# Kernel optimization log

Hardware: AMD Instinct MI355X
Metric: run time of the kernel (lower is better)

Reference implementation:

```python
import jax, jax.numpy as jnp
import numpy as np

NS = 100000   # served nodes
NI = 100000   # interfered nodes
E = 1000000   # edges per relation
D = 64        # 2 * Nt_num, Nt_num = 32
HM = 32       # message MLP hidden
HU = 16       # update MLP hidden


def _lin_init(key, fan_in, fan_out):
    s = 1.0 / np.sqrt(fan_in)
    kw, kb = jax.random.split(key)
    w = jax.random.uniform(kw, (fan_in, fan_out), jnp.float32, -s, s)
    b = jax.random.uniform(kb, (fan_out,), jnp.float32, -s, s)
    return w, b


def setup_inputs() -> dict:
    key = jax.random.key(0)
    ks = jax.random.split(key, 12)
    wm1, bm1 = _lin_init(ks[0], D, HM)
    wm2, bm2 = _lin_init(ks[1], HM, D)
    wu1, bu1 = _lin_init(ks[2], D, HU)
    wu2, bu2 = _lin_init(ks[3], HU, D)
    wo, bo = _lin_init(ks[4], D, D)
    edge_s2i = jnp.stack([
        jax.random.randint(ks[5], (E,), 0, NS),   # src in served
        jax.random.randint(ks[6], (E,), 0, NI),   # dst in interfered
    ]).astype(jnp.int64)
    edge_i2s = jnp.stack([
        jax.random.randint(ks[7], (E,), 0, NI),   # src in interfered
        jax.random.randint(ks[8], (E,), 0, NS),   # dst in served
    ]).astype(jnp.int64)
    return {
        "x_served": jax.random.normal(ks[9], (NS, D), jnp.float32),
        "x_interfered": jax.random.normal(ks[10], (NI, D), jnp.float32),
        "edge_s2i": edge_s2i,
        "edge_i2s": edge_i2s,
        "wm1": wm1, "bm1": bm1, "wm2": wm2, "bm2": bm2,
        "wu1": wu1, "bu1": bu1, "wu2": wu2, "bu2": bu2,
        "wo": wo, "bo": bo,
    }


def reference(x_served, x_interfered, edge_s2i, edge_i2s,
              wm1, bm1, wm2, bm2, wu1, bu1, wu2, bu2, wo, bo):
    def mlp_m(h):  # MLP([D, 32, D]): Lin+ReLU, Lin+ReLU
        return jax.nn.relu(jax.nn.relu(h @ wm1 + bm1) @ wm2 + bm2)

    def mlp_u(h):  # MLP([D, 16, D])
        return jax.nn.relu(jax.nn.relu(h @ wu1 + bu1) @ wu2 + bu2)

    def conv(x_src, edges, n_dst):
        # gather source node features per edge, per-edge message MLP
        msg = mlp_m(x_src[edges[0]])                    # [E, D]
        # scatter-sum into destination nodes
        agg = jax.ops.segment_sum(msg, edges[1], num_segments=n_dst)
        return mlp_u(agg)                               # [n_dst, D]

    xs, xi = x_served, x_interfered
    for _ in range(3):
        new_i = conv(xs, edge_s2i, NI)   # served -> interfered
        new_s = conv(xi, edge_i2s, NS)   # interfered -> served
        xs, xi = new_s, new_i
    # h2o on served: Lin + Tanh -> beamforming matrix
    return jnp.tanh(xs @ wo + bo)
```

## Files before the change

kernel.cpp:

```cpp
#include <hip/hip_runtime.h>
#include <hip/hip_fp16.h>
#include <math.h>

constexpr int D = 64;
constexpr int CAP = 48;
constexpr int RPB = 256;
constexpr int EPB = 4096;

typedef _Float16 half2_t __attribute__((ext_vector_type(2)));

__device__ inline float fdot2(unsigned a, unsigned b, float c){
    return __builtin_amdgcn_fdot2(__builtin_bit_cast(half2_t, a),
                                  __builtin_bit_cast(half2_t, b), c, false);
}

__device__ inline unsigned pack2(float lo, float hi){
    __half2 h = __floats2half2_rn(lo, hi);
    return *(unsigned*)&h;
}

__device__ inline void ld16u(const unsigned* base, unsigned* w){
    const uint4* p = (const uint4*)base;
    uint4 a = p[0], b = p[1], c = p[2], d = p[3];
    w[0]=a.x;  w[1]=a.y;  w[2]=a.z;  w[3]=a.w;
    w[4]=b.x;  w[5]=b.y;  w[6]=b.z;  w[7]=b.w;
    w[8]=c.x;  w[9]=c.y;  w[10]=c.z; w[11]=c.w;
    w[12]=d.x; w[13]=d.y; w[14]=d.z; w[15]=d.w;
}

__device__ inline void store_half8(__half* dst, const float* o){
    uint4 w;
    w.x = pack2(o[0], o[1]); w.y = pack2(o[2], o[3]);
    w.z = pack2(o[4], o[5]); w.w = pack2(o[6], o[7]);
    *((uint4*)dst) = w;
}

__device__ inline void load_half8(const __half* src, float* r){
    uint4 w = *((const uint4*)src);
    __half2* h = (__half2*)&w;
    float2 f0 = __half22float2(h[0]);
    float2 f1 = __half22float2(h[1]);
    float2 f2 = __half22float2(h[2]);
    float2 f3 = __half22float2(h[3]);
    r[0] = f0.x; r[1] = f0.y; r[2] = f1.x; r[3] = f1.y;
    r[4] = f2.x; r[5] = f2.y; r[6] = f3.x; r[7] = f3.y;
}


__global__ void __launch_bounds__(256) k_bucket_mlpm(
        const int* __restrict__ es2i, const int* __restrict__ ei2s, int E, int NI,
        int NBUK, int BSTRIDE,
        int* __restrict__ gcur, unsigned* __restrict__ buckets,
        const float* __restrict__ x,
        const float* __restrict__ wm1, const float* __restrict__ bm1,
        const float* __restrict__ wm2, const float* __restrict__ bm2,
        __half* __restrict__ y, int Nmlp, int nbEdge)
{
    __shared__ __align__(16) char smem[8704];
    int t = threadIdx.x;

    if ((int)blockIdx.x < nbEdge){
        int* hist = (int*)smem;
        int* base = (int*)(smem + 4096);
        for (int i = t; i < NBUK; i += 256) hist[i] = 0;
        __syncthreads();
        int e0 = blockIdx.x * EPB + t;
        int rr[16], ss[16];
        #pragma unroll
        for (int k = 0; k < 16; k++){
            int i = e0 + k*256;
            if (i < E){
                ss[k] = es2i[i];            rr[k] = es2i[E + i];
            } else if (i < 2*E){
                int j = i - E;
                ss[k] = ei2s[j];            rr[k] = NI + ei2s[E + j];
            } else rr[k] = -1;
        }
        #pragma unroll
        for (int k = 0; k < 16; k++)
            if (rr[k] >= 0) atomicAdd(&hist[rr[k] >> 8], 1);
        __syncthreads();
        for (int b = t; b < NBUK; b += 256){
            int h = hist[b];
            base[b] = h ? atomicAdd(&gcur[b], h) : 0;
        }
        __syncthreads();
        #pragma unroll
        for (int k = 0; k < 16; k++){
            if (rr[k] >= 0){
                int b = rr[k] >> 8;
                int p = atomicAdd(&base[b], 1);
                if (p < BSTRIDE)
                    buckets[(size_t)b*BSTRIDE + p] =
                        ((unsigned)(rr[k] & 255) << 24) | (unsigned)ss[k];
            }
        }
        return;
    }

    unsigned* w1p = (unsigned*)smem;
    unsigned* w2p = (unsigned*)(smem + 4096);
    float*    sb1 = (float*)(smem + 8192);
    float*    sb2 = (float*)(smem + 8320);
    for (int i = t; i < 1024; i += 256){ int kp=i>>5, j=i&31; w1p[i]=pack2(wm1[(2*kp)*32+j], wm1[(2*kp+1)*32+j]); }
    for (int i = t; i < 1024; i += 256){ int jp=i>>6, c=i&63; w2p[i]=pack2(wm2[(2*jp)*64+c], wm2[(2*jp+1)*64+c]); }
    if (t < 32) sb1[t] = bm1[t];
    if (t < 64) sb2[t] = bm2[t];
    __syncthreads();
    int n = ((int)blockIdx.x - nbEdge)*256 + t;
    if (n >= Nmlp) return;

    const float4* xp = (const float4*)(x + (size_t)n*D);
    unsigned xq[32];
    #pragma unroll
    for (int i = 0; i < 16; i++){
        float4 v = xp[i];
        xq[2*i]   = pack2(v.x, v.y);
        xq[2*i+1] = pack2(v.z, v.w);
    }
    float h[32];
    #pragma unroll
    for (int j = 0; j < 32; j++) h[j] = 0.f;
    #pragma unroll
    for (int kp = 0; kp < 32; kp++){
        unsigned xv = xq[kp];
        unsigned w[32];
        ld16u(&w1p[kp*32],      w);
        ld16u(&w1p[kp*32 + 16], w + 16);
        #pragma unroll
        for (int j = 0; j < 32; j++) h[j] = fdot2(xv, w[j], h[j]);
    }
    #pragma unroll
    for (int j = 0; j < 32; j++) h[j] = fmaxf(h[j] + sb1[j], 0.f);
    unsigned hh[16];
    #pragma unroll
    for (int jp = 0; jp < 16; jp++) hh[jp] = pack2(h[2*jp], h[2*jp+1]);

    __half* yrow = y + (size_t)n*D;
    #pragma unroll
    for (int c0 = 0; c0 < 64; c0 += 32){
        float o[32];
        #pragma unroll
        for (int c = 0; c < 32; c++) o[c] = sb2[c0 + c];
        #pragma unroll
        for (int jp = 0; jp < 16; jp++){
            unsigned hv = hh[jp];
            unsigned w[32];
            ld16u(&w2p[jp*64 + c0],      w);
            ld16u(&w2p[jp*64 + c0 + 16], w + 16);
            #pragma unroll
            for (int c = 0; c < 32; c++) o[c] = fdot2(hv, w[c], o[c]);
        }
        #pragma unroll
        for (int c = 0; c < 32; c++) o[c] = fmaxf(o[c], 0.f);
        store_half8(yrow + c0,      &o[0]);
        store_half8(yrow + c0 + 8,  &o[8]);
        store_half8(yrow + c0 + 16, &o[16]);
        store_half8(yrow + c0 + 24, &o[24]);
    }
}


__global__ void __launch_bounds__(512) k_scatter_lds(const int* __restrict__ gcur,
        const unsigned* __restrict__ buckets, int BSTRIDE, int NTOT,
        int* __restrict__ cnt, int* __restrict__ slots)
{
    __shared__ int lcnt[RPB];
    __shared__ int lslots[RPB*CAP];
    int t = threadIdx.x;
    int b = blockIdx.x;
    int r0 = b * RPB;
    int nrows = NTOT - r0; if (nrows > RPB) nrows = RPB;

    for (int i = t; i < RPB; i += 512) lcnt[i] = 0;
    __syncthreads();

    int n = gcur[b]; if (n > BSTRIDE) n = BSTRIDE;
    const unsigned* bp = buckets + (size_t)b*BSTRIDE;
    for (int k = t; k < n; k += 512){
        unsigned e = bp[k];
        int lr  = e >> 24;
        int src = e & 0xFFFFFF;
        int pos = atomicAdd(&lcnt[lr], 1);
        if (pos < CAP) lslots[lr*CAP + pos] = src;
    }
    __syncthreads();

    int4* gs = (int4*)(slots + (size_t)r0*CAP);
    const int4* ls = (const int4*)lslots;
    int n4 = nrows*CAP/4;
    for (int i = t; i < n4; i += 512) gs[i] = ls[i];
    for (int i = t; i < nrows; i += 512) cnt[r0 + i] = lcnt[i];
}


__global__ void __launch_bounds__(256) k_agg(const __half* __restrict__ M,
        const int* __restrict__ cnt, const int* __restrict__ slots,
        __half* __restrict__ agg, int N)
{
    int gid  = blockIdx.x*256 + threadIdx.x;
    int node = gid >> 6;
    if (node >= N) return;
    int lane = gid & 63;
    int sub  = lane >> 3;
    int fl   = lane & 7;
    int deg = cnt[node]; deg = deg < CAP ? deg : CAP;
    const int* row = slots + (size_t)node*CAP;
    float acc[8];
    #pragma unroll
    for (int i = 0; i < 8; i++) acc[i] = 0.f;
    for (int k = sub; k < deg; k += 8){
        int s = row[k];
        float v[8];
        load_half8(M + (size_t)s*D + fl*8, v);
        #pragma unroll
        for (int i = 0; i < 8; i++) acc[i] += v[i];
    }
    #pragma unroll
    for (int i = 0; i < 8; i++){
        acc[i] += __shfl_xor(acc[i], 8);
        acc[i] += __shfl_xor(acc[i], 16);
        acc[i] += __shfl_xor(acc[i], 32);
    }
    if (sub == 0) store_half8(agg + (size_t)node*D + fl*8, acc);
}


__global__ void __launch_bounds__(256) k_mlp_um(const __half* __restrict__ agg,
        const float* __restrict__ wu1, const float* __restrict__ bu1,
        const float* __restrict__ wu2, const float* __restrict__ bu2,
        const float* __restrict__ wm1, const float* __restrict__ bm1,
        const float* __restrict__ wm2, const float* __restrict__ bm2,
        __half* __restrict__ y, int N)
{
    __shared__ __align__(16) unsigned w1p[32*16];
    __shared__ __align__(16) unsigned w2p[8*64];
    __shared__ __align__(16) unsigned m1p[32*32];
    __shared__ __align__(16) unsigned m2p[16*64];
    __shared__ float sbu1[16], sbu2[64], sbm1[32], sbm2[64];
    int t = threadIdx.x;
    for (int i = t; i < 512;  i += 256){ int kp=i>>4, j=i&15; w1p[i]=pack2(wu1[(2*kp)*16+j], wu1[(2*kp+1)*16+j]); }
    for (int i = t; i < 512;  i += 256){ int jp=i>>6, c=i&63; w2p[i]=pack2(wu2[(2*jp)*64+c], wu2[(2*jp+1)*64+c]); }
    for (int i = t; i < 1024; i += 256){ int kp=i>>5, j=i&31; m1p[i]=pack2(wm1[(2*kp)*32+j], wm1[(2*kp+1)*32+j]); }
    for (int i = t; i < 1024; i += 256){ int kp=i>>6, c=i&63; m2p[i]=pack2(wm2[(2*kp)*64+c], wm2[(2*kp+1)*64+c]); }
    if (t < 16) sbu1[t] = bu1[t];
    if (t < 64) sbu2[t] = bu2[t];
    if (t < 32) sbm1[t] = bm1[t];
    if (t < 64) sbm2[t] = bm2[t];
    __syncthreads();
    int n = blockIdx.x*256 + t;
    if (n >= N) return;

    unsigned xq[32];
    {
        const uint4* p = (const uint4*)(agg + (size_t)n*D);
        #pragma unroll
        for (int i = 0; i < 8; i++){
            uint4 w = p[i];
            xq[4*i] = w.x; xq[4*i+1] = w.y; xq[4*i+2] = w.z; xq[4*i+3] = w.w;
        }
    }

    float h[16];
    #pragma unroll
    for (int j = 0; j < 16; j++) h[j] = 0.f;
    #pragma unroll
    for (int kp = 0; kp < 32; kp++){
        unsigned a = xq[kp];
        unsigned w[16];
        ld16u(&w1p[kp*16], w);
        #pragma unroll
        for (int j = 0; j < 16; j++) h[j] = fdot2(a, w[j], h[j]);
    }
    #pragma unroll
    for (int j = 0; j < 16; j++) h[j] = fmaxf(h[j] + sbu1[j], 0.f);
    unsigned hp[8];
    #pragma unroll
    for (int jp = 0; jp < 8; jp++) hp[jp] = pack2(h[2*jp], h[2*jp+1]);

    #pragma unroll
    for (int c0 = 0; c0 < 64; c0 += 32){
        float o[32];
        #pragma unroll
        for (int c = 0; c < 32; c++) o[c] = sbu2[c0 + c];
        #pragma unroll
        for (int jp = 0; jp < 8; jp++){
            unsigned a = hp[jp];
            unsigned w[32];
            ld16u(&w2p[jp*64 + c0],      w);
            ld16u(&w2p[jp*64 + c0 + 16], w + 16);
            #pragma unroll
            for (int c = 0; c < 32; c++) o[c] = fdot2(a, w[c], o[c]);
        }
        #pragma unroll
        for (int c = 0; c < 32; c += 2)
            xq[(c0 + c) >> 1] = pack2(fmaxf(o[c], 0.f), fmaxf(o[c+1], 0.f));
    }

    float hm[32];
    #pragma unroll
    for (int j = 0; j < 32; j++) hm[j] = 0.f;
    #pragma unroll
    for (int kp = 0; kp < 32; kp++){
        unsigned a = xq[kp];
        unsigned w[32];
        ld16u(&m1p[kp*32],      w);
        ld16u(&m1p[kp*32 + 16], w + 16);
        #pragma unroll
        for (int j = 0; j < 32; j++) hm[j] = fdot2(a, w[j], hm[j]);
    }
    #pragma unroll
    for (int j = 0; j < 32; j++) hm[j] = fmaxf(hm[j] + sbm1[j], 0.f);
    unsigned hq[16];
    #pragma unroll
    for (int jp = 0; jp < 16; jp++) hq[jp] = pack2(hm[2*jp], hm[2*jp+1]);

    __half* yrow = y + (size_t)n*D;
    #pragma unroll
    for (int c0 = 0; c0 < 64; c0 += 32){
        float o[32];
        #pragma unroll
        for (int c = 0; c < 32; c++) o[c] = sbm2[c0 + c];
        #pragma unroll
        for (int kp = 0; kp < 16; kp++){
            unsigned a = hq[kp];
            unsigned w[32];
            ld16u(&m2p[kp*64 + c0],      w);
            ld16u(&m2p[kp*64 + c0 + 16], w + 16);
            #pragma unroll
            for (int c = 0; c < 32; c++) o[c] = fdot2(a, w[c], o[c]);
        }
        #pragma unroll
        for (int c = 0; c < 32; c++) o[c] = fmaxf(o[c], 0.f);
        store_half8(yrow + c0,      &o[0]);
        store_half8(yrow + c0 + 8,  &o[8]);
        store_half8(yrow + c0 + 16, &o[16]);
        store_half8(yrow + c0 + 24, &o[24]);
    }
}


__device__ inline float fast_tanh(float x){
    float ax = fabsf(x);
    float e  = __expf(2.f*ax);
    float t  = 1.f - 2.f/(e + 1.f);
    return copysignf(t, x);
}

__global__ void __launch_bounds__(256) k_mlp_uo(const __half* __restrict__ agg,
        const float* __restrict__ wu1, const float* __restrict__ bu1,
        const float* __restrict__ wu2, const float* __restrict__ bu2,
        const float* __restrict__ wo,  const float* __restrict__ bo,
        float* __restrict__ out, int N)
{
    __shared__ __align__(16) unsigned w1p[32*16];
    __shared__ __align__(16) unsigned w2p[8*64];
    __shared__ __align__(16) unsigned wop[32*64];
    __shared__ float sbu1[16], sbu2[64], sbo[64];
    __shared__ float stage[256*65];
    int t = threadIdx.x;
    for (int i = t; i < 512;  i += 256){ int kp=i>>4, j=i&15; w1p[i]=pack2(wu1[(2*kp)*16+j], wu1[(2*kp+1)*16+j]); }
    for (int i = t; i < 512;  i += 256){ int jp=i>>6, c=i&63; w2p[i]=pack2(wu2[(2*jp)*64+c], wu2[(2*jp+1)*64+c]); }
    for (int i = t; i < 2048; i += 256){ int kp=i>>6, c=i&63; wop[i]=pack2(wo[(2*kp)*64+c], wo[(2*kp+1)*64+c]); }
    if (t < 16) sbu1[t] = bu1[t];
    if (t < 64) sbu2[t] = bu2[t];
    if (t < 64) sbo[t]  = bo[t];
    __syncthreads();
    int n = blockIdx.x*256 + t;

    if (n < N){
        unsigned xq[32];
        {
            const uint4* p = (const uint4*)(agg + (size_t)n*D);
            #pragma unroll
            for (int i = 0; i < 8; i++){
                uint4 w = p[i];
                xq[4*i] = w.x; xq[4*i+1] = w.y; xq[4*i+2] = w.z; xq[4*i+3] = w.w;
            }
        }

        float h[16];
        #pragma unroll
        for (int j = 0; j < 16; j++) h[j] = 0.f;
        #pragma unroll
        for (int kp = 0; kp < 32; kp++){
            unsigned a = xq[kp];
            unsigned w[16];
            ld16u(&w1p[kp*16], w);
            #pragma unroll
            for (int j = 0; j < 16; j++) h[j] = fdot2(a, w[j], h[j]);
        }
        #pragma unroll
        for (int j = 0; j < 16; j++) h[j] = fmaxf(h[j] + sbu1[j], 0.f);
        unsigned hp[8];
        #pragma unroll
        for (int jp = 0; jp < 8; jp++) hp[jp] = pack2(h[2*jp], h[2*jp+1]);

        #pragma unroll
        for (int c0 = 0; c0 < 64; c0 += 32){
            float o[32];
            #pragma unroll
            for (int c = 0; c < 32; c++) o[c] = sbu2[c0 + c];
            #pragma unroll
            for (int jp = 0; jp < 8; jp++){
                unsigned a = hp[jp];
                unsigned w[32];
                ld16u(&w2p[jp*64 + c0],      w);
                ld16u(&w2p[jp*64 + c0 + 16], w + 16);
                #pragma unroll
                for (int c = 0; c < 32; c++) o[c] = fdot2(a, w[c], o[c]);
            }
            #pragma unroll
            for (int c = 0; c < 32; c += 2)
                xq[(c0 + c) >> 1] = pack2(fmaxf(o[c], 0.f), fmaxf(o[c+1], 0.f));
        }

        float* srow = &stage[t*65];
        #pragma unroll
        for (int c0 = 0; c0 < 64; c0 += 32){
            float o[32];
            #pragma unroll
            for (int c = 0; c < 32; c++) o[c] = sbo[c0 + c];
            #pragma unroll
            for (int kp = 0; kp < 32; kp++){
                unsigned a = xq[kp];
                unsigned w[32];
                ld16u(&wop[kp*64 + c0],      w);
                ld16u(&wop[kp*64 + c0 + 16], w + 16);
                #pragma unroll
                for (int c = 0; c < 32; c++) o[c] = fdot2(a, w[c], o[c]);
            }
            #pragma unroll
            for (int c = 0; c < 32; c++) srow[c0 + c] = fast_tanh(o[c]);
        }
    }
    __syncthreads();

    size_t blkbase = (size_t)blockIdx.x * 256 * 64;
    size_t limit   = (size_t)N * 64;
    #pragma unroll
    for (int k = 0; k < 16; k++){
        int f = k*256 + t;
        size_t e = blkbase + (size_t)f*4;
        if (e < limit){
            int ln = f >> 4;
            int c4 = (f & 15) * 4;
            float4 v;
            v.x = stage[ln*65 + c4];
            v.y = stage[ln*65 + c4 + 1];
            v.z = stage[ln*65 + c4 + 2];
            v.w = stage[ln*65 + c4 + 3];
            *((float4*)(out + e)) = v;
        }
    }
}


extern "C" void kernel_launch(void* const* d_in, const int* in_sizes, int n_in,
                              void* d_out, int out_size, void* d_ws, size_t ws_size,
                              hipStream_t stream)
{
    const float* x_interfered = (const float*)d_in[1];
    const int*   e_s2i        = (const int*)d_in[2];
    const int*   e_i2s        = (const int*)d_in[3];
    const float* wm1 = (const float*)d_in[4];  const float* bm1 = (const float*)d_in[5];
    const float* wm2 = (const float*)d_in[6];  const float* bm2 = (const float*)d_in[7];
    const float* wu1 = (const float*)d_in[8];  const float* bu1 = (const float*)d_in[9];
    const float* wu2 = (const float*)d_in[10]; const float* bu2 = (const float*)d_in[11];
    const float* wo  = (const float*)d_in[12]; const float* bo  = (const float*)d_in[13];

    const int NS = in_sizes[0] / D;
    const int NI = in_sizes[1] / D;
    const int E  = in_sizes[2] / 2;
    const int NMAX = (NS > NI) ? NS : NI;
    const int NTOT = NI + NS;

    const int NBUK = ((NTOT - 1) >> 8) + 1;
    int avg = (2*E) / NBUK;
    const int BSTRIDE = ((2*avg) + 1023) & ~1023;

    char* p = (char*)d_ws;
    auto alloc = [&](size_t bytes) -> void* {
        void* r = (void*)p;
        p += (bytes + 255) & ~(size_t)255;
        return r;
    };
    __half*   M      = (__half*)alloc((size_t)NMAX*D*2);
    __half*   AGG    = (__half*)alloc((size_t)NMAX*D*2);
    int*      cnt    = (int*)alloc((size_t)NTOT*4);
    int*      gcur   = (int*)alloc((size_t)NBUK*4);
    int*      slots  = (int*)alloc((size_t)NTOT*CAP*4);
    unsigned* buckets= (unsigned*)alloc((size_t)NBUK*BSTRIDE*4);
    (void)ws_size; (void)n_in; (void)out_size;

    const int* cnt_i = cnt;
    const int* cnt_s = cnt + NI;
    const int* slots_i = slots;
    const int* slots_s = slots + (size_t)NI*CAP;

    hipMemsetAsync(gcur, 0, (size_t)NBUK*4, stream);

    const int nbEdge = (2*E + EPB - 1)/EPB;
    const int nbMlp  = (NI + 255)/256;
    k_bucket_mlpm<<<nbEdge + nbMlp, 256, 0, stream>>>(
        e_s2i, e_i2s, E, NI, NBUK, BSTRIDE, gcur, buckets,
        x_interfered, wm1, bm1, wm2, bm2, M, NI, nbEdge);
    k_scatter_lds<<<NBUK, 512, 0, stream>>>(gcur, buckets, BSTRIDE, NTOT, cnt, slots);

    k_agg<<<((size_t)NS*64 + 255)/256, 256, 0, stream>>>(M, cnt_s, slots_s, AGG, NS);
    k_mlp_um<<<(NS + 255)/256, 256, 0, stream>>>(AGG, wu1, bu1, wu2, bu2,
                                               wm1, bm1, wm2, bm2, M, NS);
    k_agg<<<((size_t)NI*64 + 255)/256, 256, 0, stream>>>(M, cnt_i, slots_i, AGG, NI);
    k_mlp_um<<<(NI + 255)/256, 256, 0, stream>>>(AGG, wu1, bu1, wu2, bu2,
                                               wm1, bm1, wm2, bm2, M, NI);
    k_agg<<<((size_t)NS*64 + 255)/256, 256, 0, stream>>>(M, cnt_s, slots_s, AGG, NS);
    k_mlp_uo<<<(NS + 255)/256, 256, 0, stream>>>(AGG, wu1, bu1, wu2, bu2,
                                               wo, bo, (float*)d_out, NS);
}
```

Baseline: 250.8 us.

## Use MFMA 16x16x32 f16 for fused update+message MLP kernel

Rewrites k_mlp_um so each wavefront processes 16 nodes at a time with MFMA matrix instructions instead of per-thread fdot2 loops. Weights are held in registers as MFMA B fragments, and intermediate activations go through small per-wave LDS tiles to re-layout them as A fragments. Each block now covers 128 nodes in two tiles, and the grid size is adjusted to match. This is meant to cut VALU work and LDS weight re-reads, at the cost of LDS round-trips between layers and no sync between the per-wave LDS writes and reads.

```diff
diff --git a/kernel.cpp b/kernel.cpp
--- a/kernel.cpp
+++ b/kernel.cpp
@@ -8,6 +8,8 @@
 constexpr int EPB = 4096;
 
 typedef _Float16 half2_t __attribute__((ext_vector_type(2)));
+typedef _Float16 f16x8 __attribute__((ext_vector_type(8)));
+typedef float f32x4 __attribute__((ext_vector_type(4)));
 
 __device__ inline float fdot2(unsigned a, unsigned b, float c){
     return __builtin_amdgcn_fdot2(__builtin_bit_cast(half2_t, a),
@@ -233,109 +235,121 @@
         const float* __restrict__ wm2, const float* __restrict__ bm2,
         __half* __restrict__ y, int N)
 {
-    __shared__ __align__(16) unsigned w1p[32*16];
-    __shared__ __align__(16) unsigned w2p[8*64];
-    __shared__ __align__(16) unsigned m1p[32*32];
-    __shared__ __align__(16) unsigned m2p[16*64];
-    __shared__ float sbu1[16], sbu2[64], sbm1[32], sbm2[64];
-    int t = threadIdx.x;
-    for (int i = t; i < 512;  i += 256){ int kp=i>>4, j=i&15; w1p[i]=pack2(wu1[(2*kp)*16+j], wu1[(2*kp+1)*16+j]); }
-    for (int i = t; i < 512;  i += 256){ int jp=i>>6, c=i&63; w2p[i]=pack2(wu2[(2*jp)*64+c], wu2[(2*jp+1)*64+c]); }
-    for (int i = t; i < 1024; i += 256){ int kp=i>>5, j=i&31; m1p[i]=pack2(wm1[(2*kp)*32+j], wm1[(2*kp+1)*32+j]); }
-    for (int i = t; i < 1024; i += 256){ int kp=i>>6, c=i&63; m2p[i]=pack2(wm2[(2*kp)*64+c], wm2[(2*kp+1)*64+c]); }
-    if (t < 16) sbu1[t] = bu1[t];
-    if (t < 64) sbu2[t] = bu2[t];
-    if (t < 32) sbm1[t] = bm1[t];
-    if (t < 64) sbm2[t] = bm2[t];
-    __syncthreads();
-    int n = blockIdx.x*256 + t;
-    if (n >= N) return;
-
-    unsigned xq[32];
-    {
-        const uint4* p = (const uint4*)(agg + (size_t)n*D);
+    __shared__ float  lds_h [4][16][20];
+    __shared__ float  lds_y [4][16][68];
+    __shared__ float  lds_hm[4][16][36];
+    __shared__ __half lds_m [4][16][72];
+
+    int t  = threadIdx.x;
+    int wv = t >> 6, l = t & 63;
+    int m  = l & 15, g = l >> 4;
+
+    f16x8 Bu1[2], Bu2[4], Bm1[2][2], Bm2[4];
+    #pragma unroll
+    for (int kt = 0; kt < 2; kt++)
+        #pragma unroll
+        for (int i = 0; i < 8; i++)
+            Bu1[kt][i] = (_Float16)wu1[(kt*32 + 8*g + i)*16 + m];
+    #pragma unroll
+    for (int jb = 0; jb < 4; jb++)
         #pragma unroll
         for (int i = 0; i < 8; i++){
-            uint4 w = p[i];
-            xq[4*i] = w.x; xq[4*i+1] = w.y; xq[4*i+2] = w.z; xq[4*i+3] = w.w;
-        }
-    }
-
-    float h[16];
-    #pragma unroll
-    for (int j = 0; j < 16; j++) h[j] = 0.f;
-    #pragma unroll
-    for (int kp = 0; kp < 32; kp++){
-        unsigned a = xq[kp];
-        unsigned w[16];
-        ld16u(&w1p[kp*16], w);
-        #pragma unroll
-        for (int j = 0; j < 16; j++) h[j] = fdot2(a, w[j], h[j]);
-    }
-    #pragma unroll
-    for (int j = 0; j < 16; j++) h[j] = fmaxf(h[j] + sbu1[j], 0.f);
-    unsigned hp[8];
-    #pragma unroll
-    for (int jp = 0; jp < 8; jp++) hp[jp] = pack2(h[2*jp], h[2*jp+1]);
-
-    #pragma unroll
-    for (int c0 = 0; c0 < 64; c0 += 32){
-        float o[32];
-        #pragma unroll
-        for (int c = 0; c < 32; c++) o[c] = sbu2[c0 + c];
-        #pragma unroll
-        for (int jp = 0; jp < 8; jp++){
-            unsigned a = hp[jp];
-            unsigned w[32];
-            ld16u(&w2p[jp*64 + c0],      w);
-            ld16u(&w2p[jp*64 + c0 + 16], w + 16);
-            #pragma unroll
-            for (int c = 0; c < 32; c++) o[c] = fdot2(a, w[c], o[c]);
-        }
-        #pragma unroll
-        for (int c = 0; c < 32; c += 2)
-            xq[(c0 + c) >> 1] = pack2(fmaxf(o[c], 0.f), fmaxf(o[c+1], 0.f));
-    }
-
-    float hm[32];
-    #pragma unroll
-    for (int j = 0; j < 32; j++) hm[j] = 0.f;
-    #pragma unroll
-    for (int kp = 0; kp < 32; kp++){
-        unsigned a = xq[kp];
-        unsigned w[32];
-        ld16u(&m1p[kp*32],      w);
-        ld16u(&m1p[kp*32 + 16], w + 16);
-        #pragma unroll
-        for (int j = 0; j < 32; j++) hm[j] = fdot2(a, w[j], hm[j]);
-    }
-    #pragma unroll
-    for (int j = 0; j < 32; j++) hm[j] = fmaxf(hm[j] + sbm1[j], 0.f);
-    unsigned hq[16];
-    #pragma unroll
-    for (int jp = 0; jp < 16; jp++) hq[jp] = pack2(hm[2*jp], hm[2*jp+1]);
-
-    __half* yrow = y + (size_t)n*D;
-    #pragma unroll
-    for (int c0 = 0; c0 < 64; c0 += 32){
-        float o[32];
-        #pragma unroll
-        for (int c = 0; c < 32; c++) o[c] = sbm2[c0 + c];
-        #pragma unroll
-        for (int kp = 0; kp < 16; kp++){
-            unsigned a = hq[kp];
-            unsigned w[32];
-            ld16u(&m2p[kp*64 + c0],      w);
-            ld16u(&m2p[kp*64 + c0 + 16], w + 16);
-            #pragma unroll
-            for (int c = 0; c < 32; c++) o[c] = fdot2(a, w[c], o[c]);
-        }
-        #pragma unroll
-        for (int c = 0; c < 32; c++) o[c] = fmaxf(o[c], 0.f);
-        store_half8(yrow + c0,      &o[0]);
-        store_half8(yrow + c0 + 8,  &o[8]);
-        store_half8(yrow + c0 + 16, &o[16]);
-        store_half8(yrow + c0 + 24, &o[24]);
+            int k = 8*g + i;
+            Bu2[jb][i] = (k < 16) ? (_Float16)wu2[k*64 + jb*16 + m] : (_Float16)0.f;
+        }
+    #pragma unroll
+    for (int kt = 0; kt < 2; kt++)
+        #pragma unroll
+        for (int nt = 0; nt < 2; nt++)
+            #pragma unroll
+            for (int i = 0; i < 8; i++)
+                Bm1[kt][nt][i] = (_Float16)wm1[(kt*32 + 8*g + i)*32 + nt*16 + m];
+    #pragma unroll
+    for (int jb = 0; jb < 4; jb++)
+        #pragma unroll
+        for (int i = 0; i < 8; i++)
+            Bm2[jb][i] = (_Float16)wm2[(8*g + i)*64 + jb*16 + m];
+
+    float bu1v = bu1[m];
+    float bu2v[4], bm2v[4], bm1v[2];
+    #pragma unroll
+    for (int jb = 0; jb < 4; jb++){ bu2v[jb] = bu2[jb*16 + m]; bm2v[jb] = bm2[jb*16 + m]; }
+    #pragma unroll
+    for (int nt = 0; nt < 2; nt++) bm1v[nt] = bm1[nt*16 + m];
+
+    #pragma unroll
+    for (int tile = 0; tile < 2; tile++){
+        int nb = blockIdx.x*128 + tile*64 + wv*16;
+        if (nb >= N) break;
+
+        int an = nb + m; if (an >= N) an = N - 1;
+        const __half* arow = agg + (size_t)an*64;
+        f16x8 Ax0 = *reinterpret_cast<const f16x8*>(arow + 8*g);
+        f16x8 Ax1 = *reinterpret_cast<const f16x8*>(arow + 32 + 8*g);
+
+        f32x4 acc = {0.f, 0.f, 0.f, 0.f};
+        acc = __builtin_amdgcn_mfma_f32_16x16x32_f16(Ax0, Bu1[0], acc, 0, 0, 0);
+        acc = __builtin_amdgcn_mfma_f32_16x16x32_f16(Ax1, Bu1[1], acc, 0, 0, 0);
+        #pragma unroll
+        for (int r = 0; r < 4; r++)
+            lds_h[wv][4*g + r][m] = fmaxf(acc[r] + bu1v, 0.f);
+
+        f16x8 Ah;
+        #pragma unroll
+        for (int i = 0; i < 8; i++){
+            int k = 8*g + i;
+            Ah[i] = (k < 16) ? (_Float16)lds_h[wv][m][k] : (_Float16)0.f;
+        }
+
+        #pragma unroll
+        for (int jb = 0; jb < 4; jb++){
+            f32x4 a2 = {0.f, 0.f, 0.f, 0.f};
+            a2 = __builtin_amdgcn_mfma_f32_16x16x32_f16(Ah, Bu2[jb], a2, 0, 0, 0);
+            #pragma unroll
+            for (int r = 0; r < 4; r++)
+                lds_y[wv][4*g + r][jb*16 + m] = fmaxf(a2[r] + bu2v[jb], 0.f);
+        }
+
+        f16x8 Ay0, Ay1;
+        #pragma unroll
+        for (int i = 0; i < 8; i++){
+            Ay0[i] = (_Float16)lds_y[wv][m][8*g + i];
+            Ay1[i] = (_Float16)lds_y[wv][m][32 + 8*g + i];
+        }
+
+        #pragma unroll
+        for (int nt = 0; nt < 2; nt++){
+            f32x4 a3 = {0.f, 0.f, 0.f, 0.f};
+            a3 = __builtin_amdgcn_mfma_f32_16x16x32_f16(Ay0, Bm1[0][nt], a3, 0, 0, 0);
+            a3 = __builtin_amdgcn_mfma_f32_16x16x32_f16(Ay1, Bm1[1][nt], a3, 0, 0, 0);
+            #pragma unroll
+            for (int r = 0; r < 4; r++)
+                lds_hm[wv][4*g + r][nt*16 + m] = fmaxf(a3[r] + bm1v[nt], 0.f);
+        }
+
+        f16x8 Ahm;
+        #pragma unroll
+        for (int i = 0; i < 8; i++)
+            Ahm[i] = (_Float16)lds_hm[wv][m][8*g + i];
+
+        #pragma unroll
+        for (int jb = 0; jb < 4; jb++){
+            f32x4 a4 = {0.f, 0.f, 0.f, 0.f};
+            a4 = __builtin_amdgcn_mfma_f32_16x16x32_f16(Ahm, Bm2[jb], a4, 0, 0, 0);
+            #pragma unroll
+            for (int r = 0; r < 4; r++)
+                lds_m[wv][4*g + r][jb*16 + m] = __float2half(fmaxf(a4[r] + bm2v[jb], 0.f));
+        }
+
+        int lr = l >> 2;
+        int node = nb + lr;
+        if (node < N){
+            uint4* dst = (uint4*)(y + (size_t)node*64);
+            const uint4* src = (const uint4*)&lds_m[wv][lr][0];
+            int c = l & 3;
+            dst[c]     = src[c];
+            dst[c + 4] = src[c + 4];
+        }
     }
 }
 
@@ -508,10 +522,10 @@
     k_scatter_lds<<<NBUK, 512, 0, stream>>>(gcur, buckets, BSTRIDE, NTOT, cnt, slots);
 
     k_agg<<<((size_t)NS*64 + 255)/256, 256, 0, stream>>>(M, cnt_s, slots_s, AGG, NS);
-    k_mlp_um<<<(NS + 255)/256, 256, 0, stream>>>(AGG, wu1, bu1, wu2, bu2,
+    k_mlp_um<<<(NS + 127)/128, 256, 0, stream>>>(AGG, wu1, bu1, wu2, bu2,
                                                wm1, bm1, wm2, bm2, M, NS);
     k_agg<<<((size_t)NI*64 + 255)/256, 256, 0, stream>>>(M, cnt_i, slots_i, AGG, NI);
-    k_mlp_um<<<(NI + 255)/256, 256, 0, stream>>>(AGG, wu1, bu1, wu2, bu2,
+    k_mlp_um<<<(NI + 127)/128, 256, 0, stream>>>(AGG, wu1, bu1, wu2, bu2,
                                                wm1, bm1, wm2, bm2, M, NI);
     k_agg<<<((size_t)NS*64 + 255)/256, 256, 0, stream>>>(M, cnt_s, slots_s, AGG, NS);
     k_mlp_uo<<<(NS + 255)/256, 256, 0, stream>>>(AGG, wu1, bu1, wu2, bu2,
```

Result: faster. 232.6 us (-7.3%).
